# Kernel optimization log

Hardware: AMD Instinct MI355X
Metric: run time of the kernel (lower is better)

Reference implementation:

```python
import jax, jax.numpy as jnp
import numpy as np

B = 128        # batch
N = 4096       # FLAGS.network_node
D_IN = 32      # embedding_in_size
D_OUT = 32     # embedding_out_size


def setup_inputs() -> dict:
    key = jax.random.key(0)
    k1, k2, k3, k4 = jax.random.split(key, 4)
    inputs = jax.random.normal(k1, (B, N * D_IN), dtype=jnp.float32)
    # mean-aggregation neighbor matrix: random nonneg, row-normalized (get_neibhour_nodes_matrix_mean)
    raw = jax.random.uniform(k2, (N, N), dtype=jnp.float32)
    adj = raw / jnp.sum(raw, axis=1, keepdims=True)
    # glorot uniform init as in source
    r = np.sqrt(6.0 / (D_IN + D_OUT)).astype(np.float32)
    W_neigh = jax.random.uniform(k3, (D_IN, D_OUT), minval=-r, maxval=r, dtype=jnp.float32)
    W_self = jax.random.uniform(k4, (D_IN, D_OUT), minval=-r, maxval=r, dtype=jnp.float32)
    return {"inputs": inputs, "adj": adj, "W_neigh": W_neigh, "W_self": W_self, "batch_train": 0}


def reference(inputs, adj, W_neigh, W_self, batch_train):
    # Math: relu(x @ (I_N (x) W_self + A (x) W_neigh))
    # Kronecker vec-trick: reshape x to [B, N, D_IN]; then
    #   x @ (A (x) W) reshaped = einsum('bip,ij,pq->bjq', x3, A, W)
    x3 = inputs.reshape(B, N, D_IN)
    self_part = jnp.einsum('bnp,pq->bnq', x3, W_self)            # I_N (x) W_self
    tmp = jnp.einsum('bip,pq->biq', x3, W_neigh)                  # apply small weight first
    neigh_part = jnp.einsum('biq,ij->bjq', tmp, adj)              # aggregate over graph
    out = jax.nn.relu(self_part + neigh_part)
    return out.reshape(B, N * D_OUT)
```

## Files before the change

### kernel.cpp

```cpp
#include <hip/hip_runtime.h>
#include <hip/hip_bf16.h>

#define N_NODES 4096
#define BATCH   128
#define DD      32

typedef float  f32x4  __attribute__((ext_vector_type(4)));
typedef __bf16 bf16x8 __attribute__((ext_vector_type(8)));
typedef int    i32x4  __attribute__((ext_vector_type(4)));
typedef int    i32x8  __attribute__((ext_vector_type(8)));

#define PREP_BLOCKS 2048
#define TR_BLOCKS   4096

__device__ __forceinline__ void async_copy16(const void* g, void* l) {
    __builtin_amdgcn_global_load_lds(
        (const __attribute__((address_space(1))) unsigned int*)g,
        (__attribute__((address_space(3))) unsigned int*)l,
        16, 0, 0);
}

__device__ __forceinline__ unsigned pack_fp8x4(float a, float b, float c, float d) {
    int v = __builtin_amdgcn_cvt_pk_fp8_f32(a, b, 0, false);
    v     = __builtin_amdgcn_cvt_pk_fp8_f32(c, d, v, true);
    return (unsigned)v;
}

__global__ __launch_bounds__(256) void k_pre(
    const float* __restrict__ x, const float* __restrict__ adj,
    const float* __restrict__ Wn,
    unsigned char* __restrict__ T8, unsigned char* __restrict__ adjT8)
{
    __shared__ float ts[64][65];
    const int tid = threadIdx.x;

    if (blockIdx.x < PREP_BLOCKS) {
        const int lane = tid & 63;
        const int gw   = (blockIdx.x * 256 + tid) >> 6;
        const int m    = lane & 15;
        const int quad = lane >> 4;

        bf16x8 bn[2];
#pragma unroll
        for (int h = 0; h < 2; ++h) {
            const int n = m + h * 16;
#pragma unroll
            for (int j = 0; j < 8; ++j) {
                const int k = quad * 8 + j;
                bn[h][j] = (__bf16)Wn[k * 32 + n];
            }
        }

        for (int t = gw; t < 32768; t += 8192) {
            const int row0 = t << 4;
            const int b    = row0 >> 12;
            const int i0   = row0 & 4095;

            const float4* xp = (const float4*)(x + (size_t)(row0 + m) * DD + quad * 8);
            const float4 x0 = xp[0], x1 = xp[1];
            bf16x8 a;
            a[0] = (__bf16)x0.x; a[1] = (__bf16)x0.y; a[2] = (__bf16)x0.z; a[3] = (__bf16)x0.w;
            a[4] = (__bf16)x1.x; a[5] = (__bf16)x1.y; a[6] = (__bf16)x1.z; a[7] = (__bf16)x1.w;

            const f32x4 z = {};
            const f32x4 cT0 = __builtin_amdgcn_mfma_f32_16x16x32_bf16(a, bn[0], z, 0, 0, 0);
            const f32x4 cT1 = __builtin_amdgcn_mfma_f32_16x16x32_bf16(a, bn[1], z, 0, 0, 0);

            *(unsigned*)&T8[((size_t)(b * 32 + m))      * N_NODES + i0 + quad * 4] =
                pack_fp8x4(cT0[0], cT0[1], cT0[2], cT0[3]);
            *(unsigned*)&T8[((size_t)(b * 32 + m + 16)) * N_NODES + i0 + quad * 4] =
                pack_fp8x4(cT1[0], cT1[1], cT1[2], cT1[3]);
        }
    } else {
        const int bid = blockIdx.x - PREP_BLOCKS;
        const int cx  = tid & 63;
        const int cy  = tid >> 6;
        const int i0  = (bid >> 6) << 6;
        const int j0  = (bid & 63) << 6;
#pragma unroll
        for (int r = 0; r < 16; ++r) {
            const int row = cy * 16 + r;
            ts[row][cx] = adj[(size_t)(i0 + row) * N_NODES + j0 + cx];
        }
        __syncthreads();
        const int il = (tid & 7) * 8;
        const int jb = tid >> 3;
#pragma unroll
        for (int rr = 0; rr < 2; ++rr) {
            const int jl = jb + rr * 32;
            float v[8];
#pragma unroll
            for (int k = 0; k < 8; ++k) v[k] = ts[il + k][jl] * 4096.0f;
            uint2 p;
            p.x = pack_fp8x4(v[0], v[1], v[2], v[3]);
            p.y = pack_fp8x4(v[4], v[5], v[6], v[7]);
            *(uint2*)&adjT8[(size_t)(j0 + jl) * N_NODES + i0 + il] = p;
        }
    }
}

__global__ __launch_bounds__(256) void k_gemm_neigh(
    const unsigned char* __restrict__ A8,
    const unsigned char* __restrict__ B8,
    const float* __restrict__ x,
    const float* __restrict__ Ws,
    float* __restrict__ out)
{
    __shared__ alignas(16) unsigned char As[128 * 128];
    __shared__ alignas(16) unsigned char Bs[128 * 128];

    const int tid   = threadIdx.x;
    const int lane  = tid & 63;
    const int wave  = tid >> 6;
    const int bm    = blockIdx.y << 7;
    const int bn    = blockIdx.x << 7;
    const int waveM = (wave >> 1) << 6;
    const int waveN = (wave & 1) << 6;
    const int lr    = lane & 15;
    const int lq    = lane >> 4;
    const int sw    = lr & 7;

    f32x4 acc[4][4] = {};

    const int srow = tid >> 3;
    const int scol = ((tid & 7) ^ (srow & 7)) * 16;
    const unsigned char* ga = A8 + (size_t)(bm + srow) * 4096 + scol;
    const unsigned char* gb = B8 + (size_t)(bn + srow) * 4096 + scol;
    char* la = (char*)As + tid * 16;
    char* lb = (char*)Bs + tid * 16;

    for (int k0 = 0; k0 < 4096; k0 += 128) {
#pragma unroll
        for (int n = 0; n < 4; ++n) {
            async_copy16(ga + (size_t)(n * 32) * 4096 + k0, la + n * 4096);
            async_copy16(gb + (size_t)(n * 32) * 4096 + k0, lb + n * 4096);
        }
        __syncthreads();

        i32x8 af[4], bfr[4];
#pragma unroll
        for (int t = 0; t < 4; ++t) {
            const int ra = (waveM + t * 16 + lr) * 128;
            const int rb = (waveN + t * 16 + lr) * 128;
            const int c0 = ((2 * lq)     ^ sw) * 16;
            const int c1 = ((2 * lq + 1) ^ sw) * 16;
            const i32x4 alo = *(const i32x4*)&As[ra + c0];
            const i32x4 ahi = *(const i32x4*)&As[ra + c1];
            const i32x4 blo = *(const i32x4*)&Bs[rb + c0];
            const i32x4 bhi = *(const i32x4*)&Bs[rb + c1];
            af[t][0]=alo[0]; af[t][1]=alo[1]; af[t][2]=alo[2]; af[t][3]=alo[3];
            af[t][4]=ahi[0]; af[t][5]=ahi[1]; af[t][6]=ahi[2]; af[t][7]=ahi[3];
            bfr[t][0]=blo[0]; bfr[t][1]=blo[1]; bfr[t][2]=blo[2]; bfr[t][3]=blo[3];
            bfr[t][4]=bhi[0]; bfr[t][5]=bhi[1]; bfr[t][6]=bhi[2]; bfr[t][7]=bhi[3];
        }
#pragma unroll
        for (int tm = 0; tm < 4; ++tm)
#pragma unroll
            for (int tn = 0; tn < 4; ++tn)
                acc[tm][tn] = __builtin_amdgcn_mfma_scale_f32_16x16x128_f8f6f4(
                    af[tm], bfr[tn], acc[tm][tn],
                    0, 0,
                    0, 0x7F,
                    0, 0x73);
        __syncthreads();
    }

    const f32x4 z = {};

    bf16x8 ws[2];
#pragma unroll
    for (int h = 0; h < 2; ++h)
#pragma unroll
        for (int j = 0; j < 8; ++j)
            ws[h][j] = (__bf16)Ws[(lq * 8 + j) * 32 + lr + h * 16];

    const int b0 = (bm + waveM) >> 5;
#pragma unroll
    for (int bb = 0; bb < 2; ++bb) {
        const int b = b0 + bb;
        bf16x8 xa[4];
#pragma unroll
        for (int tn = 0; tn < 4; ++tn) {
            const int gj = bn + waveN + tn * 16 + lr;
            const float4* xp = (const float4*)(x + ((size_t)b * N_NODES + gj) * DD + lq * 8);
            const float4 x0 = xp[0], x1 = xp[1];
            xa[tn][0] = (__bf16)x0.x; xa[tn][1] = (__bf16)x0.y;
            xa[tn][2] = (__bf16)x0.z; xa[tn][3] = (__bf16)x0.w;
            xa[tn][4] = (__bf16)x1.x; xa[tn][5] = (__bf16)x1.y;
            xa[tn][6] = (__bf16)x1.z; xa[tn][7] = (__bf16)x1.w;
        }
#pragma unroll
        for (int hh = 0; hh < 2; ++hh) {
            const int tm = bb * 2 + hh;
            const int q0 = hh * 16 + lq * 4;
#pragma unroll
            for (int tn = 0; tn < 4; ++tn) {
                const f32x4 u = __builtin_amdgcn_mfma_f32_16x16x32_bf16(
                    ws[hh], xa[tn], z, 0, 0, 0);
                const int gj = bn + waveN + tn * 16 + lr;
                float* p = out + (size_t)b * (N_NODES * DD) + (size_t)gj * DD + q0;
                float4 v;
                v.x = fmaxf(acc[tm][tn][0] + u[0], 0.0f);
                v.y = fmaxf(acc[tm][tn][1] + u[1], 0.0f);
                v.z = fmaxf(acc[tm][tn][2] + u[2], 0.0f);
                v.w = fmaxf(acc[tm][tn][3] + u[3], 0.0f);
                *(float4*)p = v;
            }
        }
    }
}

extern "C" void kernel_launch(void* const* d_in, const int* in_sizes, int n_in,
                              void* d_out, int out_size, void* d_ws, size_t ws_size,
                              hipStream_t stream) {
    const float* x   = (const float*)d_in[0];
    const float* adj = (const float*)d_in[1];
    const float* Wn  = (const float*)d_in[2];
    const float* Ws  = (const float*)d_in[3];
    float* out = (float*)d_out;

    unsigned char* T8    = (unsigned char*)d_ws;
    unsigned char* adjT8 = T8 + (size_t)N_NODES * N_NODES;

    hipLaunchKernelGGL(k_pre, dim3(PREP_BLOCKS + TR_BLOCKS), dim3(256), 0, stream,
                       x, adj, Wn, T8, adjT8);
    hipLaunchKernelGGL(k_gemm_neigh, dim3(32, 32), dim3(256), 0, stream,
                       T8, adjT8, x, Ws, out);
}
```

Measured before the change: 263.5 us.

## Double-buffer FP8 GEMM with 256x256 tiles, 8 waves and interleaved async loads

Replaces the single-buffered 128x128 FP8 GEMM with a 256x256 tile run by 512 threads. Shared-memory buffers are double-buffered, and the async global-to-LDS loads for the next k-steps are spread between the MFMA phases, using explicit waitcnt, barriers and setprio. Blocks are remapped so that neighbouring blocks share row and column tiles in L2. The goal is to hide load latency and raise operand reuse per byte loaded. The cost is 128 KB of LDS, more accumulator registers (8x4 per wave), and only 256 blocks, which risks low occupancy and a wave-quantisation tail.

```diff
diff --git a/kernel.cpp b/kernel.cpp
--- a/kernel.cpp
+++ b/kernel.cpp
@@ -99,74 +99,153 @@
     }
 }
 
-__global__ __launch_bounds__(256) void k_gemm_neigh(
+__global__ __launch_bounds__(512, 2) void k_gemm_neigh(
     const unsigned char* __restrict__ A8,
     const unsigned char* __restrict__ B8,
     const float* __restrict__ x,
     const float* __restrict__ Ws,
     float* __restrict__ out)
 {
-    __shared__ alignas(16) unsigned char As[128 * 128];
-    __shared__ alignas(16) unsigned char Bs[128 * 128];
+    __shared__ alignas(16) unsigned char As[2 * 256 * 128];
+    __shared__ alignas(16) unsigned char Bs[2 * 256 * 128];
 
     const int tid   = threadIdx.x;
     const int lane  = tid & 63;
-    const int wave  = tid >> 6;
-    const int bm    = blockIdx.y << 7;
-    const int bn    = blockIdx.x << 7;
-    const int waveM = (wave >> 1) << 6;
-    const int waveN = (wave & 1) << 6;
+    const int wid   = tid >> 6;
     const int lr    = lane & 15;
     const int lq    = lane >> 4;
     const int sw    = lr & 7;
-
-    f32x4 acc[4][4] = {};
-
-    const int srow = tid >> 3;
-    const int scol = ((tid & 7) ^ (srow & 7)) * 16;
-    const unsigned char* ga = A8 + (size_t)(bm + srow) * 4096 + scol;
-    const unsigned char* gb = B8 + (size_t)(bn + srow) * 4096 + scol;
-    char* la = (char*)As + tid * 16;
-    char* lb = (char*)Bs + tid * 16;
-
-    for (int k0 = 0; k0 < 4096; k0 += 128) {
-#pragma unroll
-        for (int n = 0; n < 4; ++n) {
-            async_copy16(ga + (size_t)(n * 32) * 4096 + k0, la + n * 4096);
-            async_copy16(gb + (size_t)(n * 32) * 4096 + k0, lb + n * 4096);
-        }
-        __syncthreads();
-
-        i32x8 af[4], bfr[4];
-#pragma unroll
-        for (int t = 0; t < 4; ++t) {
-            const int ra = (waveM + t * 16 + lr) * 128;
-            const int rb = (waveN + t * 16 + lr) * 128;
-            const int c0 = ((2 * lq)     ^ sw) * 16;
-            const int c1 = ((2 * lq + 1) ^ sw) * 16;
-            const i32x4 alo = *(const i32x4*)&As[ra + c0];
-            const i32x4 ahi = *(const i32x4*)&As[ra + c1];
-            const i32x4 blo = *(const i32x4*)&Bs[rb + c0];
-            const i32x4 bhi = *(const i32x4*)&Bs[rb + c1];
-            af[t][0]=alo[0]; af[t][1]=alo[1]; af[t][2]=alo[2]; af[t][3]=alo[3];
-            af[t][4]=ahi[0]; af[t][5]=ahi[1]; af[t][6]=ahi[2]; af[t][7]=ahi[3];
-            bfr[t][0]=blo[0]; bfr[t][1]=blo[1]; bfr[t][2]=blo[2]; bfr[t][3]=blo[3];
-            bfr[t][4]=bhi[0]; bfr[t][5]=bhi[1]; bfr[t][6]=bhi[2]; bfr[t][7]=bhi[3];
-        }
-#pragma unroll
-        for (int tm = 0; tm < 4; ++tm)
-#pragma unroll
-            for (int tn = 0; tn < 4; ++tn)
-                acc[tm][tn] = __builtin_amdgcn_mfma_scale_f32_16x16x128_f8f6f4(
-                    af[tm], bfr[tn], acc[tm][tn],
-                    0, 0,
-                    0, 0x7F,
-                    0, 0x73);
-        __syncthreads();
-    }
+    const int waveM = (wid >> 2) * 128;
+    const int waveN = (wid & 3) * 64;
+
+    const int wg = (blockIdx.x & 7) * 32 + (blockIdx.x >> 3);
+    const int Mb = (wg >> 4) << 8;
+    const int Nb = (wg & 15) << 8;
+
+    const int    srow  = tid >> 3;
+    const int    scol  = ((tid & 7) ^ (srow & 7)) * 16;
+    const size_t abase = (size_t)(Mb + srow) * 4096 + scol;
+    const size_t bbase = (size_t)(Nb + srow) * 4096 + scol;
+
+#define STA(bufi, r, t)                                                        \
+    async_copy16(A8 + abase + (size_t)(r) * 64 * 4096 + (t) * 128,             \
+                 (char*)As + (bufi) * 32768 + (r) * 8192 + tid * 16)
+#define STB(bufi, r, t)                                                        \
+    async_copy16(B8 + bbase + (size_t)(r) * 64 * 4096 + (t) * 128,             \
+                 (char*)Bs + (bufi) * 32768 + (r) * 8192 + tid * 16)
+#define BAR()                                                                  \
+    {                                                                          \
+        asm volatile("s_waitcnt lgkmcnt(0)" ::: "memory");                     \
+        __builtin_amdgcn_s_barrier();                                          \
+        __builtin_amdgcn_sched_barrier(0);                                     \
+    }
+
+    f32x4 acc[8][4] = {};
+
+    const int c0 = ((2 * lq)     ^ sw) * 16;
+    const int c1 = ((2 * lq + 1) ^ sw) * 16;
+
+#pragma unroll
+    for (int r = 0; r < 4; ++r) STA(0, r, 0);
+#pragma unroll
+    for (int r = 0; r < 4; ++r) STB(0, r, 0);
+#pragma unroll
+    for (int r = 0; r < 4; ++r) STB(1, r, 1);
+    STA(1, 0, 1); STA(1, 2, 1);
+    asm volatile("s_waitcnt vmcnt(6)" ::: "memory");
+    __builtin_amdgcn_s_barrier();
+    __builtin_amdgcn_sched_barrier(0);
+
+    for (int t = 0; t < 32; ++t) {
+        const int c = t & 1, o = c ^ 1;
+        const unsigned char* const cA = As + c * 32768;
+        const unsigned char* const cB = Bs + c * 32768;
+
+#define RD8(dst, base, row)                                                    \
+    {                                                                          \
+        const i32x4 _lo = *(const i32x4*)&(base)[(row) * 128 + c0];            \
+        const i32x4 _hi = *(const i32x4*)&(base)[(row) * 128 + c1];            \
+        dst[0]=_lo[0]; dst[1]=_lo[1]; dst[2]=_lo[2]; dst[3]=_lo[3];            \
+        dst[4]=_hi[0]; dst[5]=_hi[1]; dst[6]=_hi[2]; dst[7]=_hi[3];            \
+    }
+
+        i32x8 bf[4];
+#pragma unroll
+        for (int fn = 0; fn < 4; ++fn) RD8(bf[fn], cB, waveN + fn * 16 + lr);
+        i32x8 a0, a1;
+        RD8(a0, cA, waveM + 0 * 16 + lr);
+        RD8(a1, cA, waveM + 1 * 16 + lr);
+        if (t + 1 < 32) { STA(o, 1, t + 1); STA(o, 3, t + 1); }
+        __builtin_amdgcn_s_setprio(1);
+#pragma unroll
+        for (int fn = 0; fn < 4; ++fn)
+            acc[0][fn] = __builtin_amdgcn_mfma_scale_f32_16x16x128_f8f6f4(
+                a0, bf[fn], acc[0][fn], 0, 0, 0, 0x7F, 0, 0x73);
+#pragma unroll
+        for (int fn = 0; fn < 4; ++fn)
+            acc[1][fn] = __builtin_amdgcn_mfma_scale_f32_16x16x128_f8f6f4(
+                a1, bf[fn], acc[1][fn], 0, 0, 0, 0x7F, 0, 0x73);
+        __builtin_amdgcn_s_setprio(0);
+        BAR();
+
+        RD8(a0, cA, waveM + 2 * 16 + lr);
+        RD8(a1, cA, waveM + 3 * 16 + lr);
+        if (t + 2 < 32) { STB(c, 0, t + 2); STB(c, 1, t + 2);
+                          STB(c, 2, t + 2); STB(c, 3, t + 2); }
+        __builtin_amdgcn_s_setprio(1);
+#pragma unroll
+        for (int fn = 0; fn < 4; ++fn)
+            acc[2][fn] = __builtin_amdgcn_mfma_scale_f32_16x16x128_f8f6f4(
+                a0, bf[fn], acc[2][fn], 0, 0, 0, 0x7F, 0, 0x73);
+#pragma unroll
+        for (int fn = 0; fn < 4; ++fn)
+            acc[3][fn] = __builtin_amdgcn_mfma_scale_f32_16x16x128_f8f6f4(
+                a1, bf[fn], acc[3][fn], 0, 0, 0, 0x7F, 0, 0x73);
+        __builtin_amdgcn_s_setprio(0);
+        BAR();
+
+        RD8(a0, cA, waveM + 4 * 16 + lr);
+        RD8(a1, cA, waveM + 5 * 16 + lr);
+        if (t + 2 < 32) { STA(c, 0, t + 2); STA(c, 2, t + 2); }
+        __builtin_amdgcn_s_setprio(1);
+#pragma unroll
+        for (int fn = 0; fn < 4; ++fn)
+            acc[4][fn] = __builtin_amdgcn_mfma_scale_f32_16x16x128_f8f6f4(
+                a0, bf[fn], acc[4][fn], 0, 0, 0, 0x7F, 0, 0x73);
+#pragma unroll
+        for (int fn = 0; fn < 4; ++fn)
+            acc[5][fn] = __builtin_amdgcn_mfma_scale_f32_16x16x128_f8f6f4(
+                a1, bf[fn], acc[5][fn], 0, 0, 0, 0x7F, 0, 0x73);
+        __builtin_amdgcn_s_setprio(0);
+        BAR();
+
+        RD8(a0, cA, waveM + 6 * 16 + lr);
+        RD8(a1, cA, waveM + 7 * 16 + lr);
+        __builtin_amdgcn_s_setprio(1);
+#pragma unroll
+        for (int fn = 0; fn < 4; ++fn)
+            acc[6][fn] = __builtin_amdgcn_mfma_scale_f32_16x16x128_f8f6f4(
+                a0, bf[fn], acc[6][fn], 0, 0, 0, 0x7F, 0, 0x73);
+#pragma unroll
+        for (int fn = 0; fn < 4; ++fn)
+            acc[7][fn] = __builtin_amdgcn_mfma_scale_f32_16x16x128_f8f6f4(
+                a1, bf[fn], acc[7][fn], 0, 0, 0, 0x7F, 0, 0x73);
+        __builtin_amdgcn_s_setprio(0);
+        asm volatile("s_waitcnt lgkmcnt(0)" ::: "memory");
+        if (t + 2 < 32)      { asm volatile("s_waitcnt vmcnt(6)" ::: "memory"); }
+        else if (t + 1 < 32) { asm volatile("s_waitcnt vmcnt(0)" ::: "memory"); }
+        __builtin_amdgcn_sched_barrier(0);
+        if (t + 1 < 32) {
+            __builtin_amdgcn_s_barrier();
+            __builtin_amdgcn_sched_barrier(0);
+        }
+    }
+#undef RD8
+#undef STA
+#undef STB
+#undef BAR
 
     const f32x4 z = {};
-
     bf16x8 ws[2];
 #pragma unroll
     for (int h = 0; h < 2; ++h)
@@ -174,36 +253,36 @@
         for (int j = 0; j < 8; ++j)
             ws[h][j] = (__bf16)Ws[(lq * 8 + j) * 32 + lr + h * 16];
 
-    const int b0 = (bm + waveM) >> 5;
-#pragma unroll
-    for (int bb = 0; bb < 2; ++bb) {
+    const int b0 = (Mb + waveM) >> 5;
+#pragma unroll
+    for (int bb = 0; bb < 4; ++bb) {
         const int b = b0 + bb;
         bf16x8 xa[4];
 #pragma unroll
-        for (int tn = 0; tn < 4; ++tn) {
-            const int gj = bn + waveN + tn * 16 + lr;
+        for (int fn = 0; fn < 4; ++fn) {
+            const int gj = Nb + waveN + fn * 16 + lr;
             const float4* xp = (const float4*)(x + ((size_t)b * N_NODES + gj) * DD + lq * 8);
             const float4 x0 = xp[0], x1 = xp[1];
-            xa[tn][0] = (__bf16)x0.x; xa[tn][1] = (__bf16)x0.y;
-            xa[tn][2] = (__bf16)x0.z; xa[tn][3] = (__bf16)x0.w;
-            xa[tn][4] = (__bf16)x1.x; xa[tn][5] = (__bf16)x1.y;
-            xa[tn][6] = (__bf16)x1.z; xa[tn][7] = (__bf16)x1.w;
+            xa[fn][0] = (__bf16)x0.x; xa[fn][1] = (__bf16)x0.y;
+            xa[fn][2] = (__bf16)x0.z; xa[fn][3] = (__bf16)x0.w;
+            xa[fn][4] = (__bf16)x1.x; xa[fn][5] = (__bf16)x1.y;
+            xa[fn][6] = (__bf16)x1.z; xa[fn][7] = (__bf16)x1.w;
         }
 #pragma unroll
         for (int hh = 0; hh < 2; ++hh) {
-            const int tm = bb * 2 + hh;
+            const int fm = bb * 2 + hh;
             const int q0 = hh * 16 + lq * 4;
 #pragma unroll
-            for (int tn = 0; tn < 4; ++tn) {
+            for (int fn = 0; fn < 4; ++fn) {
                 const f32x4 u = __builtin_amdgcn_mfma_f32_16x16x32_bf16(
-                    ws[hh], xa[tn], z, 0, 0, 0);
-                const int gj = bn + waveN + tn * 16 + lr;
+                    ws[hh], xa[fn], z, 0, 0, 0);
+                const int gj = Nb + waveN + fn * 16 + lr;
                 float* p = out + (size_t)b * (N_NODES * DD) + (size_t)gj * DD + q0;
                 float4 v;
-                v.x = fmaxf(acc[tm][tn][0] + u[0], 0.0f);
-                v.y = fmaxf(acc[tm][tn][1] + u[1], 0.0f);
-                v.z = fmaxf(acc[tm][tn][2] + u[2], 0.0f);
-                v.w = fmaxf(acc[tm][tn][3] + u[3], 0.0f);
+                v.x = fmaxf(acc[fm][fn][0] + u[0], 0.0f);
+                v.y = fmaxf(acc[fm][fn][1] + u[1], 0.0f);
+                v.z = fmaxf(acc[fm][fn][2] + u[2], 0.0f);
+                v.w = fmaxf(acc[fm][fn][3] + u[3], 0.0f);
                 *(float4*)p = v;
             }
         }
@@ -224,6 +303,6 @@
 
     hipLaunchKernelGGL(k_pre, dim3(PREP_BLOCKS + TR_BLOCKS), dim3(256), 0, stream,
                        x, adj, Wn, T8, adjT8);
-    hipLaunchKernelGGL(k_gemm_neigh, dim3(32, 32), dim3(256), 0, stream,
+    hipLaunchKernelGGL(k_gemm_neigh, dim3(256), dim3(512), 0, stream,
                        T8, adjT8, x, Ws, out);
 }
```

After: 263.8 us. About the same (+0.1%).
